# Kernel tuning notes

Measured on AMD Instinct MI355X. Metric: run time of the kernel, lower is better.

Reference implementation:

```python
import jax, jax.numpy as jnp
import numpy as np

N_NODES = 100000
N_EDGES = 3200000
IN_F, HID_F, OUT_F = 512, 64, 16


def setup_inputs() -> dict:
    key = jax.random.key(0)
    k1, k2, k3, k4 = jax.random.split(key, 4)
    x = jax.random.normal(k1, (N_NODES, IN_F), dtype=jnp.float32)
    edge_index = jax.random.randint(k2, (2, N_EDGES), 0, N_NODES, dtype=jnp.int64)
    W1 = jax.random.normal(k3, (IN_F, HID_F), dtype=jnp.float32) * (1.0 / np.sqrt(IN_F))
    b1 = jnp.zeros((HID_F,), dtype=jnp.float32)
    W2 = jax.random.normal(k4, (HID_F, OUT_F), dtype=jnp.float32) * (1.0 / np.sqrt(HID_F))
    b2 = jnp.zeros((OUT_F,), dtype=jnp.float32)
    return {"x": x, "edge_index": edge_index, "W1": W1, "b1": b1, "W2": W2, "b2": b2}


def _gcn_norm(edge_index, n_nodes):
    # add self-loops (GCNConv default), edge_weight = 1
    loop = jnp.arange(n_nodes, dtype=edge_index.dtype)
    src = jnp.concatenate([edge_index[0], loop])
    dst = jnp.concatenate([edge_index[1], loop])
    ones = jnp.ones(src.shape[0], dtype=jnp.float32)
    deg = jax.ops.segment_sum(ones, dst, num_segments=n_nodes)
    dinv = jnp.where(deg > 0, jax.lax.rsqrt(deg), 0.0)
    norm = dinv[src] * dinv[dst]  # symmetric normalization D^-1/2 A D^-1/2
    return src, dst, norm


def _gcn_conv(h, src, dst, norm, W, b, n_nodes):
    h = h @ W                                 # project first (small GEMM)
    msg = h[src] * norm[:, None]              # gather + scale  [E+N, F_out]
    agg = jax.ops.segment_sum(msg, dst, num_segments=n_nodes)  # scatter-add
    return agg + b


def reference(x, edge_index, W1, b1, W2, b2):
    n = x.shape[0]
    src, dst, norm = _gcn_norm(edge_index, n)
    h = jax.nn.relu(_gcn_conv(x, src, dst, norm, W1, b1, n))
    # F.dropout with training=False is identity (eval-mode reference)
    h = _gcn_conv(h, src, dst, norm, W2, b2, n)
    return jax.nn.log_softmax(h, axis=1)
```

## Files before the change

kernel.cpp:

```cpp
#include <hip/hip_runtime.h>

#define NN    100000
#define NE    3200000
#define INF_  512
#define HIDF  64
#define OUTF  16
#define BR    128
#define NBUCK ((NN + BR - 1) / BR)
#define NGRP  8
#define SLICE 704
#define BSLOT (NGRP * SLICE)
#define NCUR  (NBUCK * NGRP)
#define NSLOT 72
#define EBLK  16384
#define NFB   ((NE + EBLK - 1) / EBLK)
#define GM    64
#define NGB   ((NN + GM - 1) / GM)

typedef __bf16 bf16x8 __attribute__((ext_vector_type(8)));
typedef float  f32x4  __attribute__((ext_vector_type(4)));

__device__ inline unsigned short f2bfu(float f) {
    unsigned u = __builtin_bit_cast(unsigned, f);
    u += 0x7FFFu + ((u >> 16) & 1u);
    return (unsigned short)(u >> 16);
}
__device__ inline __bf16 bfbits(unsigned short h) {
    return __builtin_bit_cast(__bf16, h);
}
__device__ inline float bf2f(unsigned short h) {
    unsigned u = (unsigned)h << 16;
    return __builtin_bit_cast(float, u);
}

__device__ inline void gll16(const float* g, void* l) {
    __builtin_amdgcn_global_load_lds(
        (const __attribute__((address_space(1))) unsigned int*)g,
        (__attribute__((address_space(3))) unsigned int*)l,
        16, 0, 0);
}

__global__ __launch_bounds__(256) void k_prep(const float* __restrict__ W1,
                                              unsigned short* __restrict__ w1c,
                                              int* __restrict__ bcur) {
    int b = blockIdx.x, t = threadIdx.x;
    if (b < 128) {
        int i = b * 256 + t;
        int k = i >> 6, n = i & 63;
        w1c[((k >> 2) * 64 + n) * 4 + (k & 3)] = f2bfu(W1[i]);
    } else {
        int i = (b - 128) * 256 + t;
        if (i < NCUR) bcur[i] = (i >> 3) * BSLOT + (i & 7) * SLICE;
    }
}

__global__ __launch_bounds__(256) void k_main(const float* __restrict__ x,
                                              const unsigned short* __restrict__ w1c,
                                              const int* __restrict__ src,
                                              const int* __restrict__ dst,
                                              int* __restrict__ bcur,
                                              unsigned int* __restrict__ pairs,
                                              unsigned short* __restrict__ h1s) {
    __shared__ __align__(16) char smem[49152];
    int t = threadIdx.x;

    if (blockIdx.x < NFB) {
        int* hist  = (int*)smem;
        int* rbase = ((int*)smem) + NBUCK;
        int e0 = blockIdx.x * EBLK;
        int e1 = (e0 + EBLK < NE) ? e0 + EBLK : NE;
        int grp = (int)(((long long)blockIdx.x * NGRP) / NFB);

        for (int b = t; b < NBUCK; b += 256) hist[b] = 0;
        __syncthreads();
        for (int e = e0 + t; e < e1; e += 256)
            atomicAdd(&hist[dst[e] >> 7], 1);
        __syncthreads();
        for (int b = t; b < NBUCK; b += 256) {
            int c = hist[b];
            rbase[b] = c ? atomicAdd(&bcur[b * NGRP + grp], c) : 0;
            hist[b] = 0;
        }
        __syncthreads();
        for (int e = e0 + t; e < e1; e += 256) {
            int s = src[e], d = dst[e];
            int b = d >> 7;
            int slot = atomicAdd(&hist[b], 1);
            pairs[rbase[b] + slot] = ((unsigned)s << 7) | (unsigned)(d & 127);
        }
        return;
    }

    unsigned short* bs = (unsigned short*)smem;
    float*          xt = (float*)(smem + 16384);
    int lane = t & 63;
    int w    = __builtin_amdgcn_readfirstlane(t >> 6);
    int m    = lane & 15;
    int kg   = lane >> 4;
    int mb   = (blockIdx.x - NFB) * GM;

    int rl_half = lane >> 5;
    int segl    = lane & 31;

    int rA = w * 16 + m;
    int swz = rA & 7;

    f32x4 acc0 = {0.f,0.f,0.f,0.f}, acc1 = acc0, acc2 = acc0, acc3 = acc0;

    const uint4* w1c4 = (const uint4*)w1c;
    uint4* bs4 = (uint4*)bs;

    for (int kc = 0; kc < 4; ++kc) {
        if (kc) __syncthreads();
#pragma unroll
        for (int i = 0; i < 4; ++i)
            bs4[t + i * 256] = w1c4[kc * 1024 + t + i * 256];
#pragma unroll
        for (int i = 0; i < 8; ++i) {
            int rloc = w * 16 + i * 2 + rl_half;
            int rg   = mb + rloc; if (rg >= NN) rg = NN - 1;
            int sseg = segl ^ (rloc & 7);
            const float* gp = x + (size_t)rg * INF_ + kc * 128 + sseg * 4;
            gll16(gp, (char*)xt + (w * 8192 + i * 1024));
        }
        __syncthreads();

#pragma unroll
        for (int ks = 0; ks < 4; ++ks) {
            int s0g = ks * 8 + kg;
            float4 xa  = *(const float4*)&xt[rA * 128 + ((s0g ^ swz) << 2)];
            float4 xbv = *(const float4*)&xt[rA * 128 + (((s0g + 4) ^ swz) << 2)];
            bf16x8 A;
            A[0] = bfbits(f2bfu(xa.x));  A[1] = bfbits(f2bfu(xa.y));
            A[2] = bfbits(f2bfu(xa.z));  A[3] = bfbits(f2bfu(xa.w));
            A[4] = bfbits(f2bfu(xbv.x)); A[5] = bfbits(f2bfu(xbv.y));
            A[6] = bfbits(f2bfu(xbv.z)); A[7] = bfbits(f2bfu(xbv.w));

            int qq0 = ks * 8 + kg;
            int qq1 = qq0 + 4;
#pragma unroll
            for (int n0t = 0; n0t < 4; ++n0t) {
                ushort4 b0 = *(const ushort4*)&bs[(qq0 * 64 + n0t * 16 + m) * 4];
                ushort4 b1 = *(const ushort4*)&bs[(qq1 * 64 + n0t * 16 + m) * 4];
                bf16x8 B;
                B[0] = bfbits(b0.x); B[1] = bfbits(b0.y);
                B[2] = bfbits(b0.z); B[3] = bfbits(b0.w);
                B[4] = bfbits(b1.x); B[5] = bfbits(b1.y);
                B[6] = bfbits(b1.z); B[7] = bfbits(b1.w);
                f32x4 c = (n0t == 0) ? acc0 : (n0t == 1) ? acc1 : (n0t == 2) ? acc2 : acc3;
                c = __builtin_amdgcn_mfma_f32_16x16x32_bf16(A, B, c, 0, 0, 0);
                if      (n0t == 0) acc0 = c;
                else if (n0t == 1) acc1 = c;
                else if (n0t == 2) acc2 = c;
                else               acc3 = c;
            }
        }
    }

#pragma unroll
    for (int r = 0; r < 4; ++r) {
        int node = mb + w * 16 + kg * 4 + r;
        if (node < NN) {
            size_t o = (size_t)node * HIDF + m;
            h1s[o +  0] = f2bfu(acc0[r]);
            h1s[o + 16] = f2bfu(acc1[r]);
            h1s[o + 32] = f2bfu(acc2[r]);
            h1s[o + 48] = f2bfu(acc3[r]);
        }
    }
}

__global__ __launch_bounds__(256) void k_fillB(const int* __restrict__ bcur,
                                               const unsigned int* __restrict__ pairs,
                                               int* __restrict__ re,
                                               float* __restrict__ dinv,
                                               int* __restrict__ csr,
                                               unsigned short* __restrict__ h1s) {
    __shared__ int   cur_s[BR];
    __shared__ float dinv_s[BR];
    int b  = blockIdx.x;
    int t  = threadIdx.x;
    int n0 = b * BR;
    int ncount = ((n0 + BR < NN) ? BR : NN - n0);

    if (t < BR) cur_s[t] = (n0 + t) * NSLOT;
    __syncthreads();

    for (int g = 0; g < NGRP; ++g) {
        int s0 = b * BSLOT + g * SLICE;
        int s1 = bcur[b * NGRP + g];
        for (int j = s0 + t; j < s1; j += 256) {
            unsigned int p = pairs[j];
            int pos = atomicAdd(&cur_s[p & 127u], 1);
            csr[pos] = (int)(p >> 7);
        }
    }
    __syncthreads();

    if (t < ncount) {
        int endp = cur_s[t];
        int n = n0 + t;
        float dv = rsqrtf((float)(endp - n * NSLOT + 1));
        re[n]    = endp;
        dinv[n]  = dv;
        dinv_s[t] = dv;
    }
    __syncthreads();

    for (int i = t; i < ncount * HIDF; i += 256) {
        unsigned idx = (unsigned)(n0 * HIDF + i);
        h1s[idx] = f2bfu(bf2f(h1s[idx]) * dinv_s[i >> 6]);
    }
}

__global__ __launch_bounds__(256) void k_hid2(const int* __restrict__ re,
                                              const int* __restrict__ csr,
                                              const float* __restrict__ dinv,
                                              const unsigned short* __restrict__ h1s,
                                              const float* __restrict__ b1,
                                              const float* __restrict__ W2,
                                              unsigned short* __restrict__ h2s) {
    __shared__ float w2s[HIDF * OUTF];
    __shared__ float b1s[HIDF];
    __shared__ float hbuf[4][HIDF];
    int t = threadIdx.x;
    for (int i = t; i < HIDF * OUTF; i += 256) w2s[i] = W2[i];
    if (t < HIDF) b1s[t] = b1[t];
    __syncthreads();

    int l = t & 63;
    int w = t >> 6;
    int g = l >> 4;
    int q = l & 15;
    int n = __builtin_amdgcn_readfirstlane(blockIdx.x * 4 + w);
    int row = n * NSLOT;
    int end = re[n];
    float dn = dinv[n];

    float a0 = 0.f, a1 = 0.f, a2 = 0.f, a3 = 0.f;

    int j = row;
    for (; j + 16 <= end; j += 16) {
        int4 scA = *(const int4*)&csr[j];
        int4 scB = *(const int4*)&csr[j + 4];
        int4 scC = *(const int4*)&csr[j + 8];
        int4 scD = *(const int4*)&csr[j + 12];
        int sA = (g & 2) ? ((g & 1) ? scA.w : scA.z) : ((g & 1) ? scA.y : scA.x);
        int sB = (g & 2) ? ((g & 1) ? scB.w : scB.z) : ((g & 1) ? scB.y : scB.x);
        int sC = (g & 2) ? ((g & 1) ? scC.w : scC.z) : ((g & 1) ? scC.y : scC.x);
        int sD = (g & 2) ? ((g & 1) ? scD.w : scD.z) : ((g & 1) ? scD.y : scD.x);
        ushort4 hA = *(const ushort4*)&h1s[(unsigned)(sA * HIDF + q * 4)];
        ushort4 hB = *(const ushort4*)&h1s[(unsigned)(sB * HIDF + q * 4)];
        ushort4 hC = *(const ushort4*)&h1s[(unsigned)(sC * HIDF + q * 4)];
        ushort4 hD = *(const ushort4*)&h1s[(unsigned)(sD * HIDF + q * 4)];
        a0 += (bf2f(hA.x) + bf2f(hB.x)) + (bf2f(hC.x) + bf2f(hD.x));
        a1 += (bf2f(hA.y) + bf2f(hB.y)) + (bf2f(hC.y) + bf2f(hD.y));
        a2 += (bf2f(hA.z) + bf2f(hB.z)) + (bf2f(hC.z) + bf2f(hD.z));
        a3 += (bf2f(hA.w) + bf2f(hB.w)) + (bf2f(hC.w) + bf2f(hD.w));
    }
    for (; j + 8 <= end; j += 8) {
        int4 scA = *(const int4*)&csr[j];
        int4 scB = *(const int4*)&csr[j + 4];
        int sA = (g & 2) ? ((g & 1) ? scA.w : scA.z) : ((g & 1) ? scA.y : scA.x);
        int sB = (g & 2) ? ((g & 1) ? scB.w : scB.z) : ((g & 1) ? scB.y : scB.x);
        ushort4 hA = *(const ushort4*)&h1s[(unsigned)(sA * HIDF + q * 4)];
        ushort4 hB = *(const ushort4*)&h1s[(unsigned)(sB * HIDF + q * 4)];
        a0 += bf2f(hA.x) + bf2f(hB.x);
        a1 += bf2f(hA.y) + bf2f(hB.y);
        a2 += bf2f(hA.z) + bf2f(hB.z);
        a3 += bf2f(hA.w) + bf2f(hB.w);
    }
    if (j + 4 <= end) {
        int4 sc = *(const int4*)&csr[j];
        int s = (g & 2) ? ((g & 1) ? sc.w : sc.z) : ((g & 1) ? sc.y : sc.x);
        ushort4 h = *(const ushort4*)&h1s[(unsigned)(s * HIDF + q * 4)];
        a0 += bf2f(h.x); a1 += bf2f(h.y); a2 += bf2f(h.z); a3 += bf2f(h.w);
        j += 4;
    }
    if (j + g < end) {
        int s = csr[j + g];
        ushort4 h = *(const ushort4*)&h1s[(unsigned)(s * HIDF + q * 4)];
        a0 += bf2f(h.x); a1 += bf2f(h.y); a2 += bf2f(h.z); a3 += bf2f(h.w);
    }

    a0 += __shfl_xor(a0, 16); a1 += __shfl_xor(a1, 16);
    a2 += __shfl_xor(a2, 16); a3 += __shfl_xor(a3, 16);
    a0 += __shfl_xor(a0, 32); a1 += __shfl_xor(a1, 32);
    a2 += __shfl_xor(a2, 32); a3 += __shfl_xor(a3, 32);

    ushort4 hs = *(const ushort4*)&h1s[(unsigned)(n * HIDF + q * 4)];
    a0 = fmaxf(fmaf(dn, a0 + bf2f(hs.x), b1s[q * 4 + 0]), 0.f);
    a1 = fmaxf(fmaf(dn, a1 + bf2f(hs.y), b1s[q * 4 + 1]), 0.f);
    a2 = fmaxf(fmaf(dn, a2 + bf2f(hs.z), b1s[q * 4 + 2]), 0.f);
    a3 = fmaxf(fmaf(dn, a3 + bf2f(hs.w), b1s[q * 4 + 3]), 0.f);
    if (g == 0) *(float4*)&hbuf[w][q * 4] = make_float4(a0, a1, a2, a3);
    __syncthreads();

    int o  = l & 15;
    int kg = l >> 4;
    const float* hb = hbuf[w];
    float s = 0.f;
#pragma unroll
    for (int i = 0; i < 16; ++i) {
        int k = kg * 16 + i;
        s = fmaf(hb[k], w2s[k * OUTF + o], s);
    }
    s += __shfl_xor(s, 16);
    s += __shfl_xor(s, 32);
    if (l < 16) h2s[(unsigned)(n * OUTF + o)] = f2bfu(dn * s);
}

__global__ __launch_bounds__(256) void k_out2(const int* __restrict__ re,
                                              const int* __restrict__ csr,
                                              const float* __restrict__ dinv,
                                              const unsigned short* __restrict__ h2s,
                                              const float* __restrict__ b2,
                                              float* __restrict__ out) {
    int t = blockIdx.x * 256 + threadIdx.x;
    int n = t >> 4;
    int f = t & 15;
    if (n >= NN) return;
    int row = n * NSLOT, end = re[n];
    float dn = dinv[n];
    float acc = bf2f(h2s[(unsigned)(n * OUTF + f)]);

    int j = row;
    for (; j + 8 <= end; j += 8) {
        int s0 = csr[j],     s1 = csr[j + 1], s2 = csr[j + 2], s3 = csr[j + 3];
        int s4 = csr[j + 4], s5 = csr[j + 5], s6 = csr[j + 6], s7 = csr[j + 7];
        float v0 = bf2f(h2s[(unsigned)(s0 * OUTF + f)]);
        float v1 = bf2f(h2s[(unsigned)(s1 * OUTF + f)]);
        float v2 = bf2f(h2s[(unsigned)(s2 * OUTF + f)]);
        float v3 = bf2f(h2s[(unsigned)(s3 * OUTF + f)]);
        float v4 = bf2f(h2s[(unsigned)(s4 * OUTF + f)]);
        float v5 = bf2f(h2s[(unsigned)(s5 * OUTF + f)]);
        float v6 = bf2f(h2s[(unsigned)(s6 * OUTF + f)]);
        float v7 = bf2f(h2s[(unsigned)(s7 * OUTF + f)]);
        acc += ((v0 + v1) + (v2 + v3)) + ((v4 + v5) + (v6 + v7));
    }
    for (; j + 4 <= end; j += 4) {
        int s0 = csr[j], s1 = csr[j + 1], s2 = csr[j + 2], s3 = csr[j + 3];
        float v0 = bf2f(h2s[(unsigned)(s0 * OUTF + f)]);
        float v1 = bf2f(h2s[(unsigned)(s1 * OUTF + f)]);
        float v2 = bf2f(h2s[(unsigned)(s2 * OUTF + f)]);
        float v3 = bf2f(h2s[(unsigned)(s3 * OUTF + f)]);
        acc += (v0 + v1) + (v2 + v3);
    }
    for (; j < end; ++j)
        acc += bf2f(h2s[(unsigned)(csr[j] * OUTF + f)]);

    float v = fmaf(dn, acc, b2[f]);

    float m = v;
#pragma unroll
    for (int mask = 1; mask < 16; mask <<= 1)
        m = fmaxf(m, __shfl_xor(m, mask, 16));
    float ex = __expf(v - m);
    float s  = ex;
#pragma unroll
    for (int mask = 1; mask < 16; mask <<= 1)
        s += __shfl_xor(s, mask, 16);
    out[(size_t)n * OUTF + f] = v - (m + __logf(s));
}

extern "C" void kernel_launch(void* const* d_in, const int* in_sizes, int n_in,
                              void* d_out, int out_size, void* d_ws, size_t ws_size,
                              hipStream_t stream) {
    const float* x  = (const float*)d_in[0];
    const int*   ei = (const int*)d_in[1];
    const float* W1 = (const float*)d_in[2];
    const float* b1 = (const float*)d_in[3];
    const float* W2 = (const float*)d_in[4];
    const float* b2 = (const float*)d_in[5];
    float*       out = (float*)d_out;

    char*  ws = (char*)d_ws;
    size_t o  = 0;
    auto alloc = [&](size_t bytes) {
        void* p = ws + o;
        o = (o + bytes + 1023) & ~(size_t)1023;
        return p;
    };
    int*            bcur  = (int*)           alloc((size_t)NCUR * 4);
    int*            re    = (int*)           alloc((size_t)NN * 4);
    int*            csr   = (int*)           alloc((size_t)NN * NSLOT * 4);
    unsigned int*   pairs = (unsigned int*)  alloc((size_t)NBUCK * BSLOT * 4);
    float*          dinv  = (float*)         alloc((size_t)NN * 4);
    unsigned short* w1c   = (unsigned short*)alloc((size_t)INF_ * HIDF * 2);
    unsigned short* h1s   = (unsigned short*)alloc((size_t)NN * HIDF * 2);
    unsigned short* h2s   = (unsigned short*)alloc((size_t)NN * OUTF * 2);
    if (o > ws_size) return;

    const int* esrc = ei;
    const int* edst = ei + NE;

    k_prep  <<<128 + (NCUR + 255) / 256, 256, 0, stream>>>(W1, w1c, bcur);
    k_main  <<<NFB + NGB, 256, 0, stream>>>(x, w1c, esrc, edst, bcur, pairs, h1s);
    k_fillB <<<NBUCK, 256, 0, stream>>>(bcur, pairs, re, dinv, csr, h1s);
    k_hid2  <<<NN / 4, 256, 0, stream>>>(re, csr, dinv, h1s, b1, W2, h2s);
    k_out2  <<<(NN * OUTF + 255) / 256, 256, 0, stream>>>(re, csr, dinv, h2s, b2, out);
}
```

Baseline: 246.7 us.

## Split the x@W1 GEMM over K across four blocks and reduce partials in fillB

The first-layer projection now launches four times as many GEMM blocks, and each handles one 128-wide K slice instead of looping over all four slices. The goal is more parallelism and no serial K loop or intra-block barriers between slices. Each block writes fp32 partial sums to a new workspace buffer of 4×N×64 floats. The fillB kernel then sums the four partials and applies the degree scaling and bf16 conversion. The trade-off is about 100 MB of extra global writes and reads for the partials.

```diff
diff --git a/kernel.cpp b/kernel.cpp
--- a/kernel.cpp
+++ b/kernel.cpp
@@ -16,6 +16,7 @@
 #define NFB   ((NE + EBLK - 1) / EBLK)
 #define GM    64
 #define NGB   ((NN + GM - 1) / GM)
+#define KSPL  4
 
 typedef __bf16 bf16x8 __attribute__((ext_vector_type(8)));
 typedef float  f32x4  __attribute__((ext_vector_type(4)));
@@ -60,7 +61,7 @@
                                               const int* __restrict__ dst,
                                               int* __restrict__ bcur,
                                               unsigned int* __restrict__ pairs,
-                                              unsigned short* __restrict__ h1s) {
+                                              float* __restrict__ part) {
     __shared__ __align__(16) char smem[49152];
     int t = threadIdx.x;
 
@@ -93,67 +94,66 @@
 
     unsigned short* bs = (unsigned short*)smem;
     float*          xt = (float*)(smem + 16384);
+    int gb   = blockIdx.x - NFB;
+    int kidx = gb & 3;
+    int mbID = gb >> 2;
     int lane = t & 63;
     int w    = __builtin_amdgcn_readfirstlane(t >> 6);
     int m    = lane & 15;
     int kg   = lane >> 4;
-    int mb   = (blockIdx.x - NFB) * GM;
+    int mb   = mbID * GM;
 
     int rl_half = lane >> 5;
     int segl    = lane & 31;
-
-    int rA = w * 16 + m;
+    int rA  = w * 16 + m;
     int swz = rA & 7;
-
-    f32x4 acc0 = {0.f,0.f,0.f,0.f}, acc1 = acc0, acc2 = acc0, acc3 = acc0;
 
     const uint4* w1c4 = (const uint4*)w1c;
     uint4* bs4 = (uint4*)bs;
 
-    for (int kc = 0; kc < 4; ++kc) {
-        if (kc) __syncthreads();
-#pragma unroll
-        for (int i = 0; i < 4; ++i)
-            bs4[t + i * 256] = w1c4[kc * 1024 + t + i * 256];
-#pragma unroll
-        for (int i = 0; i < 8; ++i) {
-            int rloc = w * 16 + i * 2 + rl_half;
-            int rg   = mb + rloc; if (rg >= NN) rg = NN - 1;
-            int sseg = segl ^ (rloc & 7);
-            const float* gp = x + (size_t)rg * INF_ + kc * 128 + sseg * 4;
-            gll16(gp, (char*)xt + (w * 8192 + i * 1024));
-        }
-        __syncthreads();
-
-#pragma unroll
-        for (int ks = 0; ks < 4; ++ks) {
-            int s0g = ks * 8 + kg;
-            float4 xa  = *(const float4*)&xt[rA * 128 + ((s0g ^ swz) << 2)];
-            float4 xbv = *(const float4*)&xt[rA * 128 + (((s0g + 4) ^ swz) << 2)];
-            bf16x8 A;
-            A[0] = bfbits(f2bfu(xa.x));  A[1] = bfbits(f2bfu(xa.y));
-            A[2] = bfbits(f2bfu(xa.z));  A[3] = bfbits(f2bfu(xa.w));
-            A[4] = bfbits(f2bfu(xbv.x)); A[5] = bfbits(f2bfu(xbv.y));
-            A[6] = bfbits(f2bfu(xbv.z)); A[7] = bfbits(f2bfu(xbv.w));
-
-            int qq0 = ks * 8 + kg;
-            int qq1 = qq0 + 4;
-#pragma unroll
-            for (int n0t = 0; n0t < 4; ++n0t) {
-                ushort4 b0 = *(const ushort4*)&bs[(qq0 * 64 + n0t * 16 + m) * 4];
-                ushort4 b1 = *(const ushort4*)&bs[(qq1 * 64 + n0t * 16 + m) * 4];
-                bf16x8 B;
-                B[0] = bfbits(b0.x); B[1] = bfbits(b0.y);
-                B[2] = bfbits(b0.z); B[3] = bfbits(b0.w);
-                B[4] = bfbits(b1.x); B[5] = bfbits(b1.y);
-                B[6] = bfbits(b1.z); B[7] = bfbits(b1.w);
-                f32x4 c = (n0t == 0) ? acc0 : (n0t == 1) ? acc1 : (n0t == 2) ? acc2 : acc3;
-                c = __builtin_amdgcn_mfma_f32_16x16x32_bf16(A, B, c, 0, 0, 0);
-                if      (n0t == 0) acc0 = c;
-                else if (n0t == 1) acc1 = c;
-                else if (n0t == 2) acc2 = c;
-                else               acc3 = c;
-            }
+#pragma unroll
+    for (int i = 0; i < 4; ++i)
+        bs4[t + i * 256] = w1c4[kidx * 1024 + t + i * 256];
+#pragma unroll
+    for (int i = 0; i < 8; ++i) {
+        int rloc = w * 16 + i * 2 + rl_half;
+        int rg   = mb + rloc; if (rg >= NN) rg = NN - 1;
+        int sseg = segl ^ (rloc & 7);
+        const float* gp = x + (size_t)rg * INF_ + kidx * 128 + sseg * 4;
+        gll16(gp, (char*)xt + (w * 8192 + i * 1024));
+    }
+    __syncthreads();
+
+    f32x4 acc0 = {0.f,0.f,0.f,0.f}, acc1 = acc0, acc2 = acc0, acc3 = acc0;
+
+#pragma unroll
+    for (int ks = 0; ks < 4; ++ks) {
+        int s0g = ks * 8 + kg;
+        float4 xa  = *(const float4*)&xt[rA * 128 + ((s0g ^ swz) << 2)];
+        float4 xbv = *(const float4*)&xt[rA * 128 + (((s0g + 4) ^ swz) << 2)];
+        bf16x8 A;
+        A[0] = bfbits(f2bfu(xa.x));  A[1] = bfbits(f2bfu(xa.y));
+        A[2] = bfbits(f2bfu(xa.z));  A[3] = bfbits(f2bfu(xa.w));
+        A[4] = bfbits(f2bfu(xbv.x)); A[5] = bfbits(f2bfu(xbv.y));
+        A[6] = bfbits(f2bfu(xbv.z)); A[7] = bfbits(f2bfu(xbv.w));
+
+        int qq0 = ks * 8 + kg;
+        int qq1 = qq0 + 4;
+#pragma unroll
+        for (int n0t = 0; n0t < 4; ++n0t) {
+            ushort4 b0 = *(const ushort4*)&bs[(qq0 * 64 + n0t * 16 + m) * 4];
+            ushort4 b1 = *(const ushort4*)&bs[(qq1 * 64 + n0t * 16 + m) * 4];
+            bf16x8 B;
+            B[0] = bfbits(b0.x); B[1] = bfbits(b0.y);
+            B[2] = bfbits(b0.z); B[3] = bfbits(b0.w);
+            B[4] = bfbits(b1.x); B[5] = bfbits(b1.y);
+            B[6] = bfbits(b1.z); B[7] = bfbits(b1.w);
+            f32x4 c = (n0t == 0) ? acc0 : (n0t == 1) ? acc1 : (n0t == 2) ? acc2 : acc3;
+            c = __builtin_amdgcn_mfma_f32_16x16x32_bf16(A, B, c, 0, 0, 0);
+            if      (n0t == 0) acc0 = c;
+            else if (n0t == 1) acc1 = c;
+            else if (n0t == 2) acc2 = c;
+            else               acc3 = c;
         }
     }
 
@@ -161,11 +161,11 @@
     for (int r = 0; r < 4; ++r) {
         int node = mb + w * 16 + kg * 4 + r;
         if (node < NN) {
-            size_t o = (size_t)node * HIDF + m;
-            h1s[o +  0] = f2bfu(acc0[r]);
-            h1s[o + 16] = f2bfu(acc1[r]);
-            h1s[o + 32] = f2bfu(acc2[r]);
-            h1s[o + 48] = f2bfu(acc3[r]);
+            size_t o = ((size_t)kidx * NN + node) * HIDF + m;
+            part[o +  0] = acc0[r];
+            part[o + 16] = acc1[r];
+            part[o + 32] = acc2[r];
+            part[o + 48] = acc3[r];
         }
     }
 }
@@ -175,6 +175,7 @@
                                                int* __restrict__ re,
                                                float* __restrict__ dinv,
                                                int* __restrict__ csr,
+                                               const float* __restrict__ part,
                                                unsigned short* __restrict__ h1s) {
     __shared__ int   cur_s[BR];
     __shared__ float dinv_s[BR];
@@ -208,8 +209,10 @@
     __syncthreads();
 
     for (int i = t; i < ncount * HIDF; i += 256) {
-        unsigned idx = (unsigned)(n0 * HIDF + i);
-        h1s[idx] = f2bfu(bf2f(h1s[idx]) * dinv_s[i >> 6]);
+        size_t idx = (size_t)n0 * HIDF + i;
+        float v = (part[idx] + part[(size_t)NN * HIDF + idx])
+                + (part[2 * (size_t)NN * HIDF + idx] + part[3 * (size_t)NN * HIDF + idx]);
+        h1s[idx] = f2bfu(v * dinv_s[i >> 6]);
     }
 }
 
@@ -387,6 +390,7 @@
     unsigned int*   pairs = (unsigned int*)  alloc((size_t)NBUCK * BSLOT * 4);
     float*          dinv  = (float*)         alloc((size_t)NN * 4);
     unsigned short* w1c   = (unsigned short*)alloc((size_t)INF_ * HIDF * 2);
+    float*          part  = (float*)         alloc((size_t)KSPL * NN * HIDF * 4);
     unsigned short* h1s   = (unsigned short*)alloc((size_t)NN * HIDF * 2);
     unsigned short* h2s   = (unsigned short*)alloc((size_t)NN * OUTF * 2);
     if (o > ws_size) return;
@@ -395,8 +399,8 @@
     const int* edst = ei + NE;
 
     k_prep  <<<128 + (NCUR + 255) / 256, 256, 0, stream>>>(W1, w1c, bcur);
-    k_main  <<<NFB + NGB, 256, 0, stream>>>(x, w1c, esrc, edst, bcur, pairs, h1s);
-    k_fillB <<<NBUCK, 256, 0, stream>>>(bcur, pairs, re, dinv, csr, h1s);
+    k_main  <<<NFB + KSPL * NGB, 256, 0, stream>>>(x, w1c, esrc, edst, bcur, pairs, part);
+    k_fillB <<<NBUCK, 256, 0, stream>>>(bcur, pairs, re, dinv, csr, part, h1s);
     k_hid2  <<<NN / 4, 256, 0, stream>>>(re, csr, dinv, h1s, b1, W2, h2s);
     k_out2  <<<(NN * OUTF + 255) / 256, 256, 0, stream>>>(re, csr, dinv, h2s, b2, out);
 }
```

Result: slower. 268.3 us (+8.7%).
